# Kernel optimization log

Measured on AMD Instinct MI355X. Metric: run time of the kernel, lower is better.

The kernel has to match this reference:

```python
import jax, jax.numpy as jnp
import numpy as np

B, N, C, H = 4, 1024, 768, 12
D = C // H  # head_dim = 64


def setup_inputs() -> dict:
    key = jax.random.key(0)
    ks = jax.random.split(key, 16)
    def lin(k, fan_in, fan_out):
        # torch Linear init: U(-1/sqrt(fan_in), 1/sqrt(fan_in)); stored as [in, out]
        bound = 1.0 / np.sqrt(fan_in)
        kw, kb = jax.random.split(k)
        W = jax.random.uniform(kw, (fan_in, fan_out), minval=-bound, maxval=bound, dtype=jnp.float32)
        b = jax.random.uniform(kb, (fan_out,), minval=-bound, maxval=bound, dtype=jnp.float32)
        return W, b
    Wq, bq = lin(ks[0], C, C)
    Wk, bk = lin(ks[1], C, C)
    Wv, bv = lin(ks[2], C, C)
    Wo, bo = lin(ks[3], C, C)
    Wd1, bd1 = lin(ks[4], 1, 16)
    Wd2, bd2 = lin(ks[5], 16, H)
    x = jax.random.normal(ks[6], (B, N, C), dtype=jnp.float32)
    coords = jax.random.uniform(ks[7], (B, N, 2), dtype=jnp.float32)
    return {"x": x, "coords": coords,
            "Wq": Wq, "bq": bq, "Wk": Wk, "bk": bk, "Wv": Wv, "bv": bv,
            "Wo": Wo, "bo": bo, "Wd1": Wd1, "bd1": bd1, "Wd2": Wd2, "bd2": bd2}


def reference(x, coords, Wq, bq, Wk, bk, Wv, bv, Wo, bo, Wd1, bd1, Wd2, bd2):
    scale = D ** (-0.5)
    # projections -> [B, H, N, D]
    def heads(t):
        return t.reshape(B, N, H, D).transpose(0, 2, 1, 3)
    q = heads(x @ Wq + bq)
    k = heads(x @ Wk + bk)
    v = heads(x @ Wv + bv)
    # content scores [B, H, N, N]
    content = jnp.einsum('bhid,bhjd->bhij', q, k) * scale
    # pairwise distances [B, N, N, 1]
    diff = coords[:, :, None, :] - coords[:, None, :, :]
    dist = jnp.sqrt(jnp.sum(diff * diff, axis=-1, keepdims=True) + 1e-6)
    # distance MLP: 1 -> 16 -> H, then permute to [B, H, N, N]
    hbias = jax.nn.relu(dist @ Wd1 + bd1)
    spatial = (hbias @ Wd2 + bd2).transpose(0, 3, 1, 2)
    attn = jax.nn.softmax(content + spatial, axis=-1)
    out = jnp.einsum('bhij,bhjd->bhid', attn, v)
    out = out.transpose(0, 2, 1, 3).reshape(B, N, C)
    out = out @ Wo + bo
    return out, attn
```

## Files before the change

### kernel.cpp

```cpp
#include <hip/hip_runtime.h>
#include <cstddef>
#include <cstdint>

#define Bc 4
#define Nc 1024
#define Cc 768
#define Hc 12
#define Dc 64
#define BHc 48
#define QKV_ELEMS ((size_t)Bc * Nc * Cc)

typedef __attribute__((ext_vector_type(4))) unsigned int u32x4;
typedef __attribute__((ext_vector_type(8))) short s16x8;
typedef __attribute__((ext_vector_type(4))) float fx4;
typedef __attribute__((ext_vector_type(2))) float fx2;

union Frag { u32x4 u; s16x8 s; unsigned short h[8]; };

__device__ inline unsigned short f2bf(float x) {
    union { float f; uint32_t u; } c; c.f = x;
    return (unsigned short)((c.u + 0x7FFFu + ((c.u >> 16) & 1u)) >> 16);
}
__device__ inline float bf2f(unsigned short b) {
    union { uint32_t u; float f; } c; c.u = ((uint32_t)b) << 16;
    return c.f;
}
__device__ inline void split8(const float* v, u32x4& hi, u32x4& lo) {
    Frag fh, fl;
    #pragma unroll
    for (int e = 0; e < 8; ++e) {
        const unsigned short hb = f2bf(v[e]);
        fh.h[e] = hb;
        fl.h[e] = f2bf(v[e] - bf2f(hb));
    }
    hi = fh.u; lo = fl.u;
}

__global__ __launch_bounds__(256) void prep_w_kernel(
    const float* __restrict__ Wq, const float* __restrict__ Wk,
    const float* __restrict__ Wv, const float* __restrict__ Wo,
    unsigned short* __restrict__ Thi, unsigned short* __restrict__ Tlo)
{
    __shared__ float scr[64 * 65];
    const int mat = blockIdx.z;
    const float* W = (mat == 0) ? Wq : (mat == 1) ? Wk : (mat == 2) ? Wv : Wo;
    const int k0 = blockIdx.y * 64, n0 = blockIdx.x * 64;
    const int tid = threadIdx.x;

    #pragma unroll
    for (int it = 0; it < 4; ++it) {
        const int lin = tid + it * 256;
        const int r = lin >> 4, c4 = (lin & 15) << 2;
        const fx4 v = *(const fx4*)&W[(size_t)(k0 + r) * 768 + n0 + c4];
        scr[r * 65 + c4 + 0] = v[0]; scr[r * 65 + c4 + 1] = v[1];
        scr[r * 65 + c4 + 2] = v[2]; scr[r * 65 + c4 + 3] = v[3];
    }
    __syncthreads();
    unsigned short* th = Thi + (size_t)mat * 768 * 768;
    unsigned short* tl = Tlo + (size_t)mat * 768 * 768;
    #pragma unroll
    for (int it = 0; it < 16; ++it) {
        const int lin = tid + it * 256;
        const int n = lin >> 6, kq = lin & 63;
        const float val = scr[kq * 65 + n];
        const size_t o = (size_t)(n0 + n) * 768 + k0 + kq;
        const unsigned short hb = f2bf(val);
        th[o] = hb;
        tl[o] = f2bf(val - bf2f(hb));
    }
}

__global__ __launch_bounds__(256) void prep_tables_kernel(
    const float* __restrict__ Wd1, const float* __restrict__ bd1,
    const float* __restrict__ Wd2, const float* __restrict__ bd2,
    float* __restrict__ abPack, float* __restrict__ kact, int* __restrict__ meta)
{
    __shared__ float w1s[16], b1s[16], kn[16];
    __shared__ int rank[16];
    const int tid = threadIdx.x;
    if (tid < 16) {
        const float w1 = Wd1[tid], b1 = bd1[tid];
        w1s[tid] = w1; b1s[tid] = b1;
        kn[tid] = (w1 != 0.0f) ? (-b1 / w1) : INFINITY;
    }
    __syncthreads();
    if (tid < 16) {
        int rk = 0;
        for (int u = 0; u < 16; ++u) {
            const float ku = kn[u], km = kn[tid];
            if (ku < km || (ku == km && u < tid)) ++rk;
        }
        rank[tid] = rk;
    }
    if (tid == 0) {
        int nn = 0, na = 0;
        for (int t = 0; t < 16; ++t) {
            const float kt = kn[t];
            if (kt < 0.00099f) ++nn;
            else if (kt < 1.41422f) kact[na++] = kt;
        }
        meta[0] = nn; meta[1] = na;
    }
    __syncthreads();
    if (tid < 17 * 12) {
        const int s = tid / 12, h = tid % 12;
        float a = 0.0f, be = bd2[h];
        for (int u = 0; u < 16; ++u) {
            const float w1 = w1s[u], b1 = b1s[u];
            bool act;
            if (w1 > 0.0f)      act = (rank[u] < s);
            else if (w1 < 0.0f) act = (rank[u] >= s);
            else                act = (b1 > 0.0f);
            if (act) {
                const float w2 = Wd2[u * 12 + h];
                a  += w2 * w1;
                be += w2 * b1;
            }
        }
        abPack[tid * 2 + 0] = a;
        abPack[tid * 2 + 1] = be;
    }
}

__global__ __launch_bounds__(256) void split_x_kernel(
    const float* __restrict__ x, unsigned short* __restrict__ xhi,
    unsigned short* __restrict__ xlo)
{
    const size_t t = (size_t)blockIdx.x * 256 + threadIdx.x;
    float vv[8];
    const fx4 a = *(const fx4*)&x[t * 8];
    const fx4 b = *(const fx4*)&x[t * 8 + 4];
    vv[0]=a[0]; vv[1]=a[1]; vv[2]=a[2]; vv[3]=a[3];
    vv[4]=b[0]; vv[5]=b[1]; vv[6]=b[2]; vv[7]=b[3];
    u32x4 hi, lo; split8(vv, hi, lo);
    *(u32x4*)&xhi[t * 8] = hi;
    *(u32x4*)&xlo[t * 8] = lo;
}

struct SmemG { u32x4 ah[512]; u32x4 al[512]; u32x4 bh[512]; u32x4 bl[512]; };
struct SmemT { float scr[64 * 68]; };
union SmemU { SmemG g; SmemT t; };

template<int AMODE, int OMODE>
__global__ __launch_bounds__(256) void gemm_mfma_kernel(
    const unsigned short* __restrict__ Ahi, const unsigned short* __restrict__ Alo,
    const float* __restrict__ P0, const float* __restrict__ P1,
    const unsigned short* __restrict__ Bhi, const unsigned short* __restrict__ Blo,
    const float* __restrict__ bias,
    float* __restrict__ outF,
    unsigned short* __restrict__ Ohi, unsigned short* __restrict__ Olo)
{
    __shared__ SmemU sm;
    const int tid = threadIdx.x;
    const int w = tid >> 6, L = tid & 63;
    const int Lr = L & 15, Lg = L >> 4;
    const int m0 = blockIdx.y * 64, n0 = blockIdx.x * 64;

    fx4 acc[2][2] = {};

    for (int kk = 0; kk < 768; kk += 64) {
        #pragma unroll
        for (int it = 0; it < 2; ++it) {
            const int slot = tid + it * 256;
            const int s = slot >> 6, l = slot & 63;
            const int row = m0 + ((s >> 1) << 4) + (l & 15);
            const int kb = kk + ((s & 1) << 5) + ((l >> 4) << 3);
            if (AMODE == 1) {
                sm.g.ah[slot] = *(const u32x4*)&Ahi[(size_t)row * 768 + kb];
                sm.g.al[slot] = *(const u32x4*)&Alo[(size_t)row * 768 + kb];
            } else {
                const fx4 a0 = *(const fx4*)&P0[(size_t)row * 768 + kb];
                const fx4 a1 = *(const fx4*)&P0[(size_t)row * 768 + kb + 4];
                const fx4 c0 = *(const fx4*)&P1[(size_t)row * 768 + kb];
                const fx4 c1 = *(const fx4*)&P1[(size_t)row * 768 + kb + 4];
                float vv[8];
                vv[0]=a0[0]+c0[0]; vv[1]=a0[1]+c0[1]; vv[2]=a0[2]+c0[2]; vv[3]=a0[3]+c0[3];
                vv[4]=a1[0]+c1[0]; vv[5]=a1[1]+c1[1]; vv[6]=a1[2]+c1[2]; vv[7]=a1[3]+c1[3];
                u32x4 hi, lo; split8(vv, hi, lo);
                sm.g.ah[slot] = hi;
                sm.g.al[slot] = lo;
            }
            const int col = n0 + ((s >> 1) << 4) + (l & 63 & 15);
            sm.g.bh[slot] = *(const u32x4*)&Bhi[(size_t)col * 768 + kb];
            sm.g.bl[slot] = *(const u32x4*)&Blo[(size_t)col * 768 + kb];
        }
        __syncthreads();
        #pragma unroll
        for (int kc = 0; kc < 2; ++kc) {
            Frag ah[2], al[2], bh[2], bl[2];
            #pragma unroll
            for (int mm = 0; mm < 2; ++mm) {
                const int rg = (w >> 1) * 2 + mm;
                ah[mm].u = sm.g.ah[(rg * 2 + kc) * 64 + L];
                al[mm].u = sm.g.al[(rg * 2 + kc) * 64 + L];
            }
            #pragma unroll
            for (int nn = 0; nn < 2; ++nn) {
                const int cg = (w & 1) * 2 + nn;
                bh[nn].u = sm.g.bh[(cg * 2 + kc) * 64 + L];
                bl[nn].u = sm.g.bl[(cg * 2 + kc) * 64 + L];
            }
            #pragma unroll
            for (int mm = 0; mm < 2; ++mm)
                #pragma unroll
                for (int nn = 0; nn < 2; ++nn) {
                    acc[mm][nn] = __builtin_amdgcn_mfma_f32_16x16x32_bf16(ah[mm].s, bh[nn].s, acc[mm][nn], 0, 0, 0);
                    acc[mm][nn] = __builtin_amdgcn_mfma_f32_16x16x32_bf16(ah[mm].s, bl[nn].s, acc[mm][nn], 0, 0, 0);
                    acc[mm][nn] = __builtin_amdgcn_mfma_f32_16x16x32_bf16(al[mm].s, bh[nn].s, acc[mm][nn], 0, 0, 0);
                }
        }
        __syncthreads();
    }

    #pragma unroll
    for (int mm = 0; mm < 2; ++mm) {
        const int rl = (w >> 1) * 32 + mm * 16 + Lg * 4;
        #pragma unroll
        for (int nn = 0; nn < 2; ++nn) {
            const int cl = (w & 1) * 32 + nn * 16 + Lr;
            const float bs = bias[n0 + cl];
            #pragma unroll
            for (int r = 0; r < 4; ++r)
                sm.t.scr[(rl + r) * 68 + cl] = acc[mm][nn][r] + bs;
        }
    }
    __syncthreads();

    if (OMODE == 0) {
        const int h = n0 >> 6;
        #pragma unroll
        for (int it = 0; it < 2; ++it) {
            const int t = tid + it * 256;
            const int r = t >> 3, d0 = (t & 7) << 3;
            float vv[8];
            #pragma unroll
            for (int e = 0; e < 8; ++e) vv[e] = sm.t.scr[r * 68 + d0 + e];
            u32x4 hi, lo; split8(vv, hi, lo);
            const int rg = m0 + r, b = rg >> 10, nloc = rg & 1023;
            const size_t o = (((size_t)(b * Hc + h) * Nc + nloc) << 6) + d0;
            *(u32x4*)&Ohi[o] = hi;
            *(u32x4*)&Olo[o] = lo;
        }
    } else if (OMODE == 1) {
        const int b = m0 >> 10, h = n0 >> 6, nbase = m0 & 1023;
        #pragma unroll
        for (int it = 0; it < 2; ++it) {
            const int t = tid + it * 256;
            const int dd = t >> 3, j0 = (t & 7) << 3;
            float vv[8];
            #pragma unroll
            for (int e = 0; e < 8; ++e) vv[e] = sm.t.scr[(j0 + e) * 68 + dd];
            u32x4 hi, lo; split8(vv, hi, lo);
            const size_t o = (size_t)((b * Hc + h) * Dc + dd) * Nc + nbase + j0;
            *(u32x4*)&Ohi[o] = hi;
            *(u32x4*)&Olo[o] = lo;
        }
    } else {
        #pragma unroll
        for (int it = 0; it < 4; ++it) {
            const int lin = tid + it * 256;
            const int r = lin >> 4, c4 = (lin & 15) << 2;
            const fx4 v = *(const fx4*)&sm.t.scr[r * 68 + c4];
            *(fx4*)&outF[(size_t)(m0 + r) * 768 + n0 + c4] = v;
        }
    }
}

__global__ __launch_bounds__(256, 4) void scores_half_kernel(
    const unsigned short* __restrict__ qhi, const unsigned short* __restrict__ qlo,
    const unsigned short* __restrict__ khi, const unsigned short* __restrict__ klo,
    const float* __restrict__ coords,
    const float* __restrict__ abPack, const float* __restrict__ kact,
    const int* __restrict__ meta,
    float* __restrict__ attn, float* __restrict__ ml)
{
    __shared__ u32x4 KsH[512], KsL[512];
    __shared__ fx2 cjs[512];
    __shared__ fx2 abt[17];
    __shared__ float kacts[16];
    __shared__ int metas[2];

    const int tid = threadIdx.x;
    const int w = tid >> 6, L = tid & 63;
    const int Lr = L & 15, Lg = L >> 4;
    const int bh = blockIdx.z, b = bh / Hc, h = bh % Hc;
    const int i0 = blockIdx.x * 64, half = blockIdx.y;
    const int i = i0 + w * 16 + Lr;
    const int Lg4 = Lg * 4;

    if (tid < 17) abt[tid] = *(const fx2*)&abPack[(tid * Hc + h) * 2];
    else if (tid >= 32 && tid < 48) kacts[tid - 32] = kact[tid - 32];
    else if (tid == 64) { metas[0] = meta[0]; metas[1] = meta[1]; }
    for (int t = tid; t < 512; t += 256)
        cjs[t] = *(const fx2*)&coords[((size_t)b * Nc + half * 512 + t) * 2];

    Frag qh[2], ql[2];
    #pragma unroll
    for (int kc = 0; kc < 2; ++kc) {
        const size_t o = ((size_t)bh * Nc + i) * 64 + kc * 32 + Lg * 8;
        qh[kc].u = *(const u32x4*)&qhi[o];
        ql[kc].u = *(const u32x4*)&qlo[o];
    }
    const fx2 ci = *(const fx2*)&coords[((size_t)b * Nc + i) * 2];
    __syncthreads();
    const int n_neg = metas[0], n_act = metas[1];

    float m_r = -INFINITY, l_r = 0.f;
    const size_t rowbase = ((size_t)bh * Nc + i) * Nc + half * 512;

    for (int jt = 0; jt < 8; ++jt) {
        #pragma unroll
        for (int it = 0; it < 2; ++it) {
            const int slot = tid + it * 256;
            const int s = slot >> 6, l = slot & 63;
            const int jrow = half * 512 + jt * 64 + ((s >> 1) << 4) + (l & 15);
            const int kb = ((s & 1) << 5) + ((l >> 4) << 3);
            const size_t o = ((size_t)bh * Nc + jrow) * 64 + kb;
            KsH[slot] = *(const u32x4*)&khi[o];
            KsL[slot] = *(const u32x4*)&klo[o];
        }
        __syncthreads();

        fx4 acc[4] = {};
        #pragma unroll
        for (int kc = 0; kc < 2; ++kc) {
            #pragma unroll
            for (int cg = 0; cg < 4; ++cg) {
                Frag kh_, kl_;
                kh_.u = KsH[(cg * 2 + kc) * 64 + L];
                kl_.u = KsL[(cg * 2 + kc) * 64 + L];
                acc[cg] = __builtin_amdgcn_mfma_f32_16x16x32_bf16(kh_.s, qh[kc].s, acc[cg], 0, 0, 0);
                acc[cg] = __builtin_amdgcn_mfma_f32_16x16x32_bf16(kl_.s, qh[kc].s, acc[cg], 0, 0, 0);
                acc[cg] = __builtin_amdgcn_mfma_f32_16x16x32_bf16(kh_.s, ql[kc].s, acc[cg], 0, 0, 0);
            }
        }

        float sv[16];
        #pragma unroll
        for (int cg = 0; cg < 4; ++cg) {
            float dist4[4]; int idx4[4];
            #pragma unroll
            for (int r = 0; r < 4; ++r) {
                const fx2 cj = cjs[jt * 64 + cg * 16 + Lg4 + r];
                const float dx = ci[0] - cj[0], dy = ci[1] - cj[1];
                dist4[r] = sqrtf(fmaf(dx, dx, fmaf(dy, dy, 1e-6f)));
                idx4[r] = n_neg;
            }
            for (int t = 0; t < n_act; ++t) {
                const float kt = kacts[t];
                #pragma unroll
                for (int r = 0; r < 4; ++r) idx4[r] += (dist4[r] > kt) ? 1 : 0;
            }
            #pragma unroll
            for (int r = 0; r < 4; ++r) {
                const fx2 ab = abt[idx4[r]];
                sv[cg * 4 + r] = fmaf(acc[cg][r], 0.125f, fmaf(ab[0], dist4[r], ab[1]));
            }
        }

        #pragma unroll
        for (int cg = 0; cg < 4; ++cg) {
            fx4 st;
            st[0] = sv[cg*4+0]; st[1] = sv[cg*4+1]; st[2] = sv[cg*4+2]; st[3] = sv[cg*4+3];
            *(fx4*)&attn[rowbase + jt * 64 + cg * 16 + Lg4] = st;
        }

        float tm = sv[0];
        #pragma unroll
        for (int e = 1; e < 16; ++e) tm = fmaxf(tm, sv[e]);
        tm = fmaxf(tm, __shfl_xor(tm, 16));
        tm = fmaxf(tm, __shfl_xor(tm, 32));
        const float mnew = fmaxf(m_r, tm);
        float ts = 0.f;
        #pragma unroll
        for (int e = 0; e < 16; ++e) ts += __expf(sv[e] - mnew);
        ts += __shfl_xor(ts, 16);
        ts += __shfl_xor(ts, 32);
        l_r = l_r * __expf(m_r - mnew) + ts;
        m_r = mnew;
        __syncthreads();
    }

    if (Lg == 0) {
        const size_t mo = (((size_t)bh * Nc + i) * 2 + half) * 2;
        ml[mo + 0] = m_r;
        ml[mo + 1] = l_r;
    }
}

__global__ __launch_bounds__(256, 4) void pv_half_kernel(
    float* __restrict__ attn,
    const unsigned short* __restrict__ vThi, const unsigned short* __restrict__ vTlo,
    const float* __restrict__ ml,
    float* __restrict__ Hp)
{
    __shared__ u32x4 VsH[512], VsL[512];
    const int tid = threadIdx.x;
    const int w = tid >> 6, L = tid & 63;
    const int Lr = L & 15, Lg = L >> 4;
    const int bh = blockIdx.z, b = bh / Hc, h = bh % Hc;
    const int i0 = blockIdx.x * 64, half = blockIdx.y;
    const int wrow = i0 + w * 16;

    const size_t prow = (size_t)bh * Nc + wrow + Lr;
    const fx4 m4 = *(const fx4*)&ml[prow * 4];
    const float mm = fmaxf(m4[0], m4[2]);
    const float ll = m4[1] * __expf(m4[0] - mm) + m4[3] * __expf(m4[2] - mm);
    const float il = 1.0f / ll;

    fx4 acc[4] = {};

    for (int jt = 0; jt < 8; ++jt) {
        const int jglob = half * 8 + jt;
        #pragma unroll
        for (int it = 0; it < 2; ++it) {
            const int slot = tid + it * 256;
            const int s = slot >> 6, l = slot & 63;
            const int dd = ((s >> 1) << 4) + (l & 15);
            const int j = jglob * 64 + ((s & 1) << 5) + ((l >> 4) << 3);
            const size_t o = ((size_t)bh * Dc + dd) * Nc + j;
            VsH[slot] = *(const u32x4*)&vThi[o];
            VsL[slot] = *(const u32x4*)&vTlo[o];
        }
        __syncthreads();

        #pragma unroll
        for (int kc = 0; kc < 2; ++kc) {
            float* ap = &attn[prow * Nc + jglob * 64 + kc * 32 + Lg * 8];
            const fx4 s0 = *(const fx4*)ap;
            const fx4 s1 = *(const fx4*)(ap + 4);
            float p[8];
            p[0] = __expf(s0[0] - mm) * il; p[1] = __expf(s0[1] - mm) * il;
            p[2] = __expf(s0[2] - mm) * il; p[3] = __expf(s0[3] - mm) * il;
            p[4] = __expf(s1[0] - mm) * il; p[5] = __expf(s1[1] - mm) * il;
            p[6] = __expf(s1[2] - mm) * il; p[7] = __expf(s1[3] - mm) * il;
            fx4 w0, w1;
            w0[0]=p[0]; w0[1]=p[1]; w0[2]=p[2]; w0[3]=p[3];
            w1[0]=p[4]; w1[1]=p[5]; w1[2]=p[6]; w1[3]=p[7];
            *(fx4*)ap = w0;
            *(fx4*)(ap + 4) = w1;
            u32x4 phi, plo; split8(p, phi, plo);
            Frag ph, pl; ph.u = phi; pl.u = plo;
            #pragma unroll
            for (int dg = 0; dg < 4; ++dg) {
                Frag vh, vl;
                vh.u = VsH[(dg * 2 + kc) * 64 + L];
                vl.u = VsL[(dg * 2 + kc) * 64 + L];
                acc[dg] = __builtin_amdgcn_mfma_f32_16x16x32_bf16(ph.s, vh.s, acc[dg], 0, 0, 0);
                acc[dg] = __builtin_amdgcn_mfma_f32_16x16x32_bf16(ph.s, vl.s, acc[dg], 0, 0, 0);
                acc[dg] = __builtin_amdgcn_mfma_f32_16x16x32_bf16(pl.s, vh.s, acc[dg], 0, 0, 0);
            }
        }
        __syncthreads();
    }

    #pragma unroll
    for (int dg = 0; dg < 4; ++dg)
        #pragma unroll
        for (int r = 0; r < 4; ++r) {
            const int irow = wrow + Lg * 4 + r;
            Hp[(size_t)half * QKV_ELEMS + ((size_t)b * Nc + irow) * Cc + h * Dc + dg * 16 + Lr]
                = acc[dg][r];
        }
}

extern "C" void kernel_launch(void* const* d_in, const int* in_sizes, int n_in,
                              void* d_out, int out_size, void* d_ws, size_t ws_size,
                              hipStream_t stream)
{
    (void)in_sizes; (void)n_in; (void)out_size; (void)ws_size;

    const float* x      = (const float*)d_in[0];
    const float* coords = (const float*)d_in[1];
    const float* Wq = (const float*)d_in[2];  const float* bq = (const float*)d_in[3];
    const float* Wk = (const float*)d_in[4];  const float* bk = (const float*)d_in[5];
    const float* Wv = (const float*)d_in[6];  const float* bv = (const float*)d_in[7];
    const float* Wo = (const float*)d_in[8];  const float* bo = (const float*)d_in[9];
    const float* Wd1 = (const float*)d_in[10]; const float* bd1 = (const float*)d_in[11];
    const float* Wd2 = (const float*)d_in[12]; const float* bd2 = (const float*)d_in[13];

    float* out_main = (float*)d_out;
    float* attn     = out_main + QKV_ELEMS;

    uint8_t* wsb = (uint8_t*)d_ws;
    const size_t SZ_BF = (size_t)BHc * Nc * Dc * 2;
    const size_t SZ_W4 = (size_t)4 * 768 * 768 * 2;
    unsigned short* qhi  = (unsigned short*)(wsb + 0 * SZ_BF);
    unsigned short* qlo  = (unsigned short*)(wsb + 1 * SZ_BF);
    unsigned short* khi  = (unsigned short*)(wsb + 2 * SZ_BF);
    unsigned short* klo  = (unsigned short*)(wsb + 3 * SZ_BF);
    unsigned short* vThi = (unsigned short*)(wsb + 4 * SZ_BF);
    unsigned short* vTlo = (unsigned short*)(wsb + 5 * SZ_BF);
    float*          Hp   = (float*)(wsb + 0 * SZ_BF);
    unsigned short* xhi  = (unsigned short*)(wsb + 6 * SZ_BF);
    unsigned short* xlo  = (unsigned short*)(wsb + 7 * SZ_BF);
    unsigned short* Thi  = (unsigned short*)(wsb + 8 * SZ_BF);
    unsigned short* Tlo  = (unsigned short*)(wsb + 8 * SZ_BF + SZ_W4);
    float* mlbuf  = (float*)(wsb + 8 * SZ_BF + 2 * SZ_W4);
    float* abPack = mlbuf + (size_t)BHc * Nc * 4;
    float* kact   = abPack + 17 * 12 * 2;
    int*   meta   = (int*)(kact + 16);

    prep_w_kernel<<<dim3(12, 12, 4), 256, 0, stream>>>(Wq, Wk, Wv, Wo, Thi, Tlo);
    prep_tables_kernel<<<1, 256, 0, stream>>>(Wd1, bd1, Wd2, bd2, abPack, kact, meta);
    split_x_kernel<<<dim3(1536), 256, 0, stream>>>(x, xhi, xlo);

    dim3 gGemm(12, 64);
    gemm_mfma_kernel<1, 0><<<gGemm, 256, 0, stream>>>(
        xhi, xlo, nullptr, nullptr, Thi + (size_t)0 * 768 * 768, Tlo + (size_t)0 * 768 * 768,
        bq, nullptr, qhi, qlo);
    gemm_mfma_kernel<1, 0><<<gGemm, 256, 0, stream>>>(
        xhi, xlo, nullptr, nullptr, Thi + (size_t)1 * 768 * 768, Tlo + (size_t)1 * 768 * 768,
        bk, nullptr, khi, klo);
    gemm_mfma_kernel<1, 1><<<gGemm, 256, 0, stream>>>(
        xhi, xlo, nullptr, nullptr, Thi + (size_t)2 * 768 * 768, Tlo + (size_t)2 * 768 * 768,
        bv, nullptr, vThi, vTlo);

    scores_half_kernel<<<dim3(16, 2, 48), 256, 0, stream>>>(
        qhi, qlo, khi, klo, coords, abPack, kact, meta, attn, mlbuf);

    pv_half_kernel<<<dim3(16, 2, 48), 256, 0, stream>>>(
        attn, vThi, vTlo, mlbuf, Hp);

    gemm_mfma_kernel<2, 2><<<gGemm, 256, 0, stream>>>(
        nullptr, nullptr, Hp, Hp + QKV_ELEMS, Thi + (size_t)3 * 768 * 768,
        Tlo + (size_t)3 * 768 * 768, bo, out_main, nullptr, nullptr);
}
```

Measured before the change: 404.6 us.

## Store per-tile exponentials, LUT spline bins, and reduce PV halves in-block

The scores kernel now writes exp(s - tile_max) with per-64-column tile max and sum stats instead of raw scores. The pv kernel then only rescales by a per-tile factor, which removes its exp work. Spline segment lookup is replaced by a 2048-entry byte LUT built in the prep kernel, and K/V tiles are loaded directly into registers instead of staged through LDS. The PV kernel combines its two column halves in shared memory and writes a bf16 hi/lo split of the head output, so the output GEMM loads split operands directly. Risks are LUT binning errors near knot boundaries and less memory reuse without LDS staging.

```diff
diff --git a/kernel.cpp b/kernel.cpp
--- a/kernel.cpp
+++ b/kernel.cpp
@@ -73,7 +73,7 @@
 __global__ __launch_bounds__(256) void prep_tables_kernel(
     const float* __restrict__ Wd1, const float* __restrict__ bd1,
     const float* __restrict__ Wd2, const float* __restrict__ bd2,
-    float* __restrict__ abPack, float* __restrict__ kact, int* __restrict__ meta)
+    float* __restrict__ abPack, unsigned char* __restrict__ lut)
 {
     __shared__ float w1s[16], b1s[16], kn[16];
     __shared__ int rank[16];
@@ -91,15 +91,6 @@
             if (ku < km || (ku == km && u < tid)) ++rk;
         }
         rank[tid] = rk;
-    }
-    if (tid == 0) {
-        int nn = 0, na = 0;
-        for (int t = 0; t < 16; ++t) {
-            const float kt = kn[t];
-            if (kt < 0.00099f) ++nn;
-            else if (kt < 1.41422f) kact[na++] = kt;
-        }
-        meta[0] = nn; meta[1] = na;
     }
     __syncthreads();
     if (tid < 17 * 12) {
@@ -120,6 +111,12 @@
         abPack[tid * 2 + 0] = a;
         abPack[tid * 2 + 1] = be;
     }
+    for (int b = tid; b < 2048; b += 256) {
+        const float rep = (b + 0.5f) * (1.41422f / 2048.0f);
+        int cnt = 0;
+        for (int t = 0; t < 16; ++t) cnt += (rep > kn[t]) ? 1 : 0;
+        lut[b] = (unsigned char)cnt;
+    }
 }
 
 __global__ __launch_bounds__(256) void split_x_kernel(
@@ -141,10 +138,9 @@
 struct SmemT { float scr[64 * 68]; };
 union SmemU { SmemG g; SmemT t; };
 
-template<int AMODE, int OMODE>
+template<int OMODE>
 __global__ __launch_bounds__(256) void gemm_mfma_kernel(
     const unsigned short* __restrict__ Ahi, const unsigned short* __restrict__ Alo,
-    const float* __restrict__ P0, const float* __restrict__ P1,
     const unsigned short* __restrict__ Bhi, const unsigned short* __restrict__ Blo,
     const float* __restrict__ bias,
     float* __restrict__ outF,
@@ -165,22 +161,9 @@
             const int s = slot >> 6, l = slot & 63;
             const int row = m0 + ((s >> 1) << 4) + (l & 15);
             const int kb = kk + ((s & 1) << 5) + ((l >> 4) << 3);
-            if (AMODE == 1) {
-                sm.g.ah[slot] = *(const u32x4*)&Ahi[(size_t)row * 768 + kb];
-                sm.g.al[slot] = *(const u32x4*)&Alo[(size_t)row * 768 + kb];
-            } else {
-                const fx4 a0 = *(const fx4*)&P0[(size_t)row * 768 + kb];
-                const fx4 a1 = *(const fx4*)&P0[(size_t)row * 768 + kb + 4];
-                const fx4 c0 = *(const fx4*)&P1[(size_t)row * 768 + kb];
-                const fx4 c1 = *(const fx4*)&P1[(size_t)row * 768 + kb + 4];
-                float vv[8];
-                vv[0]=a0[0]+c0[0]; vv[1]=a0[1]+c0[1]; vv[2]=a0[2]+c0[2]; vv[3]=a0[3]+c0[3];
-                vv[4]=a1[0]+c1[0]; vv[5]=a1[1]+c1[1]; vv[6]=a1[2]+c1[2]; vv[7]=a1[3]+c1[3];
-                u32x4 hi, lo; split8(vv, hi, lo);
-                sm.g.ah[slot] = hi;
-                sm.g.al[slot] = lo;
-            }
-            const int col = n0 + ((s >> 1) << 4) + (l & 63 & 15);
+            sm.g.ah[slot] = *(const u32x4*)&Ahi[(size_t)row * 768 + kb];
+            sm.g.al[slot] = *(const u32x4*)&Alo[(size_t)row * 768 + kb];
+            const int col = n0 + ((s >> 1) << 4) + (l & 15);
             sm.g.bh[slot] = *(const u32x4*)&Bhi[(size_t)col * 768 + kb];
             sm.g.bl[slot] = *(const u32x4*)&Blo[(size_t)col * 768 + kb];
         }
@@ -266,19 +249,16 @@
     }
 }
 
-__global__ __launch_bounds__(256, 4) void scores_half_kernel(
+__global__ __launch_bounds__(256) void scores_kernel(
     const unsigned short* __restrict__ qhi, const unsigned short* __restrict__ qlo,
     const unsigned short* __restrict__ khi, const unsigned short* __restrict__ klo,
     const float* __restrict__ coords,
-    const float* __restrict__ abPack, const float* __restrict__ kact,
-    const int* __restrict__ meta,
-    float* __restrict__ attn, float* __restrict__ ml)
-{
-    __shared__ u32x4 KsH[512], KsL[512];
+    const float* __restrict__ abPack, const unsigned char* __restrict__ lutg,
+    float* __restrict__ attn, float* __restrict__ mlf)
+{
+    __shared__ fx2 abt[17];
+    __shared__ unsigned char luts[2048];
     __shared__ fx2 cjs[512];
-    __shared__ fx2 abt[17];
-    __shared__ float kacts[16];
-    __shared__ int metas[2];
 
     const int tid = threadIdx.x;
     const int w = tid >> 6, L = tid & 63;
@@ -288,11 +268,12 @@
     const int i = i0 + w * 16 + Lr;
     const int Lg4 = Lg * 4;
 
-    if (tid < 17) abt[tid] = *(const fx2*)&abPack[(tid * Hc + h) * 2];
-    else if (tid >= 32 && tid < 48) kacts[tid - 32] = kact[tid - 32];
-    else if (tid == 64) { metas[0] = meta[0]; metas[1] = meta[1]; }
-    for (int t = tid; t < 512; t += 256)
+    if (tid < 17) abt[tid] = ((const fx2*)abPack)[tid * Hc + h];
+    #pragma unroll
+    for (int t = tid; t < 512; t += 256) {
+        ((uint32_t*)luts)[t] = ((const uint32_t*)lutg)[t];
         cjs[t] = *(const fx2*)&coords[((size_t)b * Nc + half * 512 + t) * 2];
+    }
 
     Frag qh[2], ql[2];
     #pragma unroll
@@ -303,165 +284,163 @@
     }
     const fx2 ci = *(const fx2*)&coords[((size_t)b * Nc + i) * 2];
     __syncthreads();
-    const int n_neg = metas[0], n_act = metas[1];
-
-    float m_r = -INFINITY, l_r = 0.f;
+
     const size_t rowbase = ((size_t)bh * Nc + i) * Nc + half * 512;
+    const size_t mlbase = ((size_t)bh * Nc + i) * 16 + half * 8;
 
     for (int jt = 0; jt < 8; ++jt) {
-        #pragma unroll
-        for (int it = 0; it < 2; ++it) {
-            const int slot = tid + it * 256;
-            const int s = slot >> 6, l = slot & 63;
-            const int jrow = half * 512 + jt * 64 + ((s >> 1) << 4) + (l & 15);
-            const int kb = ((s & 1) << 5) + ((l >> 4) << 3);
-            const size_t o = ((size_t)bh * Nc + jrow) * 64 + kb;
-            KsH[slot] = *(const u32x4*)&khi[o];
-            KsL[slot] = *(const u32x4*)&klo[o];
-        }
-        __syncthreads();
+        const int jbase = half * 512 + jt * 64;
 
         fx4 acc[4] = {};
         #pragma unroll
         for (int kc = 0; kc < 2; ++kc) {
+            Frag kh[4], kl[4];
             #pragma unroll
             for (int cg = 0; cg < 4; ++cg) {
-                Frag kh_, kl_;
-                kh_.u = KsH[(cg * 2 + kc) * 64 + L];
-                kl_.u = KsL[(cg * 2 + kc) * 64 + L];
-                acc[cg] = __builtin_amdgcn_mfma_f32_16x16x32_bf16(kh_.s, qh[kc].s, acc[cg], 0, 0, 0);
-                acc[cg] = __builtin_amdgcn_mfma_f32_16x16x32_bf16(kl_.s, qh[kc].s, acc[cg], 0, 0, 0);
-                acc[cg] = __builtin_amdgcn_mfma_f32_16x16x32_bf16(kh_.s, ql[kc].s, acc[cg], 0, 0, 0);
+                const size_t o = ((size_t)bh * Nc + jbase + cg * 16 + Lr) * 64 + kc * 32 + Lg * 8;
+                kh[cg].u = *(const u32x4*)&khi[o];
+                kl[cg].u = *(const u32x4*)&klo[o];
+            }
+            #pragma unroll
+            for (int cg = 0; cg < 4; ++cg) {
+                acc[cg] = __builtin_amdgcn_mfma_f32_16x16x32_bf16(kh[cg].s, qh[kc].s, acc[cg], 0, 0, 0);
+                acc[cg] = __builtin_amdgcn_mfma_f32_16x16x32_bf16(kl[cg].s, qh[kc].s, acc[cg], 0, 0, 0);
+                acc[cg] = __builtin_amdgcn_mfma_f32_16x16x32_bf16(kh[cg].s, ql[kc].s, acc[cg], 0, 0, 0);
             }
         }
 
         float sv[16];
         #pragma unroll
         for (int cg = 0; cg < 4; ++cg) {
-            float dist4[4]; int idx4[4];
             #pragma unroll
             for (int r = 0; r < 4; ++r) {
                 const fx2 cj = cjs[jt * 64 + cg * 16 + Lg4 + r];
                 const float dx = ci[0] - cj[0], dy = ci[1] - cj[1];
-                dist4[r] = sqrtf(fmaf(dx, dx, fmaf(dy, dy, 1e-6f)));
-                idx4[r] = n_neg;
-            }
-            for (int t = 0; t < n_act; ++t) {
-                const float kt = kacts[t];
-                #pragma unroll
-                for (int r = 0; r < 4; ++r) idx4[r] += (dist4[r] > kt) ? 1 : 0;
-            }
-            #pragma unroll
-            for (int r = 0; r < 4; ++r) {
-                const fx2 ab = abt[idx4[r]];
-                sv[cg * 4 + r] = fmaf(acc[cg][r], 0.125f, fmaf(ab[0], dist4[r], ab[1]));
-            }
-        }
-
+                const float dist = sqrtf(fmaf(dx, dx, fmaf(dy, dy, 1e-6f)));
+                int bin = (int)(dist * (2048.0f / 1.41422f));
+                bin = (bin > 2047) ? 2047 : bin;
+                const fx2 ab = abt[luts[bin]];
+                sv[cg * 4 + r] = fmaf(acc[cg][r], 0.125f, fmaf(ab[0], dist, ab[1]));
+            }
+        }
+
+        float tm = sv[0];
+        #pragma unroll
+        for (int e = 1; e < 16; ++e) tm = fmaxf(tm, sv[e]);
+        tm = fmaxf(tm, __shfl_xor(tm, 16));
+        tm = fmaxf(tm, __shfl_xor(tm, 32));
+
+        float ts = 0.f;
+        #pragma unroll
+        for (int e = 0; e < 16; ++e) { sv[e] = __expf(sv[e] - tm); ts += sv[e]; }
         #pragma unroll
         for (int cg = 0; cg < 4; ++cg) {
             fx4 st;
             st[0] = sv[cg*4+0]; st[1] = sv[cg*4+1]; st[2] = sv[cg*4+2]; st[3] = sv[cg*4+3];
             *(fx4*)&attn[rowbase + jt * 64 + cg * 16 + Lg4] = st;
         }
-
-        float tm = sv[0];
-        #pragma unroll
-        for (int e = 1; e < 16; ++e) tm = fmaxf(tm, sv[e]);
-        tm = fmaxf(tm, __shfl_xor(tm, 16));
-        tm = fmaxf(tm, __shfl_xor(tm, 32));
-        const float mnew = fmaxf(m_r, tm);
-        float ts = 0.f;
-        #pragma unroll
-        for (int e = 0; e < 16; ++e) ts += __expf(sv[e] - mnew);
         ts += __shfl_xor(ts, 16);
         ts += __shfl_xor(ts, 32);
-        l_r = l_r * __expf(m_r - mnew) + ts;
-        m_r = mnew;
-        __syncthreads();
-    }
-
-    if (Lg == 0) {
-        const size_t mo = (((size_t)bh * Nc + i) * 2 + half) * 2;
-        ml[mo + 0] = m_r;
-        ml[mo + 1] = l_r;
-    }
-}
-
-__global__ __launch_bounds__(256, 4) void pv_half_kernel(
+        if (Lg == 0) {
+            *(fx2*)&mlf[(mlbase + jt) * 2] = fx2{tm, ts};
+        }
+    }
+}
+
+__global__ __launch_bounds__(256) void pv_kernel(
     float* __restrict__ attn,
     const unsigned short* __restrict__ vThi, const unsigned short* __restrict__ vTlo,
-    const float* __restrict__ ml,
-    float* __restrict__ Hp)
-{
-    __shared__ u32x4 VsH[512], VsL[512];
+    const float* __restrict__ mlf,
+    unsigned short* __restrict__ Hphi, unsigned short* __restrict__ Hplo)
+{
+    __shared__ float accs[32 * 64];
     const int tid = threadIdx.x;
     const int w = tid >> 6, L = tid & 63;
     const int Lr = L & 15, Lg = L >> 4;
-    const int bh = blockIdx.z, b = bh / Hc, h = bh % Hc;
-    const int i0 = blockIdx.x * 64, half = blockIdx.y;
-    const int wrow = i0 + w * 16;
-
-    const size_t prow = (size_t)bh * Nc + wrow + Lr;
-    const fx4 m4 = *(const fx4*)&ml[prow * 4];
-    const float mm = fmaxf(m4[0], m4[2]);
-    const float ll = m4[1] * __expf(m4[0] - mm) + m4[3] * __expf(m4[2] - mm);
-    const float il = 1.0f / ll;
+    const int wr = w >> 1, wc = w & 1;
+    const int bh = blockIdx.y, b = bh / Hc, h = bh % Hc;
+    const int i0 = blockIdx.x * 32;
+    const int row = i0 + wr * 16 + Lr;
+
+    const float* mlr = &mlf[((size_t)bh * Nc + row) * 32];
+    float mt[16], lt[16];
+    #pragma unroll
+    for (int t = 0; t < 8; ++t) {
+        const fx4 v = *(const fx4*)&mlr[t * 4];
+        mt[t*2+0] = v[0]; lt[t*2+0] = v[1];
+        mt[t*2+1] = v[2]; lt[t*2+1] = v[3];
+    }
+    float m_row = mt[0];
+    #pragma unroll
+    for (int t = 1; t < 16; ++t) m_row = fmaxf(m_row, mt[t]);
+    float l_row = 0.f;
+    #pragma unroll
+    for (int t = 0; t < 16; ++t) l_row = fmaf(lt[t], __expf(mt[t] - m_row), l_row);
+    const float il = 1.0f / l_row;
 
     fx4 acc[4] = {};
+    const size_t arow = ((size_t)bh * Nc + row) * Nc;
 
     for (int jt = 0; jt < 8; ++jt) {
-        const int jglob = half * 8 + jt;
-        #pragma unroll
-        for (int it = 0; it < 2; ++it) {
-            const int slot = tid + it * 256;
-            const int s = slot >> 6, l = slot & 63;
-            const int dd = ((s >> 1) << 4) + (l & 15);
-            const int j = jglob * 64 + ((s & 1) << 5) + ((l >> 4) << 3);
-            const size_t o = ((size_t)bh * Dc + dd) * Nc + j;
-            VsH[slot] = *(const u32x4*)&vThi[o];
-            VsL[slot] = *(const u32x4*)&vTlo[o];
-        }
-        __syncthreads();
-
+        const int jbase = wc * 512 + jt * 64;
+        const float f = __expf(mlr[(wc * 8 + jt) * 2] - m_row) * il;
         #pragma unroll
         for (int kc = 0; kc < 2; ++kc) {
-            float* ap = &attn[prow * Nc + jglob * 64 + kc * 32 + Lg * 8];
+            float* ap = &attn[arow + jbase + kc * 32 + Lg * 8];
             const fx4 s0 = *(const fx4*)ap;
             const fx4 s1 = *(const fx4*)(ap + 4);
             float p[8];
-            p[0] = __expf(s0[0] - mm) * il; p[1] = __expf(s0[1] - mm) * il;
-            p[2] = __expf(s0[2] - mm) * il; p[3] = __expf(s0[3] - mm) * il;
-            p[4] = __expf(s1[0] - mm) * il; p[5] = __expf(s1[1] - mm) * il;
-            p[6] = __expf(s1[2] - mm) * il; p[7] = __expf(s1[3] - mm) * il;
+            p[0]=s0[0]*f; p[1]=s0[1]*f; p[2]=s0[2]*f; p[3]=s0[3]*f;
+            p[4]=s1[0]*f; p[5]=s1[1]*f; p[6]=s1[2]*f; p[7]=s1[3]*f;
             fx4 w0, w1;
             w0[0]=p[0]; w0[1]=p[1]; w0[2]=p[2]; w0[3]=p[3];
             w1[0]=p[4]; w1[1]=p[5]; w1[2]=p[6]; w1[3]=p[7];
             *(fx4*)ap = w0;
             *(fx4*)(ap + 4) = w1;
-            u32x4 phi, plo; split8(p, phi, plo);
-            Frag ph, pl; ph.u = phi; pl.u = plo;
+            u32x4 phiu, plou; split8(p, phiu, plou);
+            Frag ph, pl; ph.u = phiu; pl.u = plou;
+
+            Frag vh[4], vl[4];
             #pragma unroll
             for (int dg = 0; dg < 4; ++dg) {
-                Frag vh, vl;
-                vh.u = VsH[(dg * 2 + kc) * 64 + L];
-                vl.u = VsL[(dg * 2 + kc) * 64 + L];
-                acc[dg] = __builtin_amdgcn_mfma_f32_16x16x32_bf16(ph.s, vh.s, acc[dg], 0, 0, 0);
-                acc[dg] = __builtin_amdgcn_mfma_f32_16x16x32_bf16(ph.s, vl.s, acc[dg], 0, 0, 0);
-                acc[dg] = __builtin_amdgcn_mfma_f32_16x16x32_bf16(pl.s, vh.s, acc[dg], 0, 0, 0);
-            }
-        }
-        __syncthreads();
-    }
-
-    #pragma unroll
-    for (int dg = 0; dg < 4; ++dg)
-        #pragma unroll
-        for (int r = 0; r < 4; ++r) {
-            const int irow = wrow + Lg * 4 + r;
-            Hp[(size_t)half * QKV_ELEMS + ((size_t)b * Nc + irow) * Cc + h * Dc + dg * 16 + Lr]
-                = acc[dg][r];
-        }
+                const size_t o = ((size_t)bh * Dc + dg * 16 + Lr) * Nc + jbase + kc * 32 + Lg * 8;
+                vh[dg].u = *(const u32x4*)&vThi[o];
+                vl[dg].u = *(const u32x4*)&vTlo[o];
+            }
+            #pragma unroll
+            for (int dg = 0; dg < 4; ++dg) {
+                acc[dg] = __builtin_amdgcn_mfma_f32_16x16x32_bf16(ph.s, vh[dg].s, acc[dg], 0, 0, 0);
+                acc[dg] = __builtin_amdgcn_mfma_f32_16x16x32_bf16(ph.s, vl[dg].s, acc[dg], 0, 0, 0);
+                acc[dg] = __builtin_amdgcn_mfma_f32_16x16x32_bf16(pl.s, vh[dg].s, acc[dg], 0, 0, 0);
+            }
+        }
+    }
+
+    if (wc == 0) {
+        #pragma unroll
+        for (int dg = 0; dg < 4; ++dg)
+            #pragma unroll
+            for (int r = 0; r < 4; ++r)
+                accs[(wr * 16 + Lg * 4 + r) * 64 + dg * 16 + Lr] = acc[dg][r];
+    }
+    __syncthreads();
+    if (wc == 1) {
+        #pragma unroll
+        for (int dg = 0; dg < 4; ++dg)
+            #pragma unroll
+            for (int r = 0; r < 4; ++r)
+                accs[(wr * 16 + Lg * 4 + r) * 64 + dg * 16 + Lr] += acc[dg][r];
+    }
+    __syncthreads();
+
+    const int r2 = tid >> 3, d0 = (tid & 7) << 3;
+    float vv[8];
+    #pragma unroll
+    for (int e = 0; e < 8; ++e) vv[e] = accs[r2 * 64 + d0 + e];
+    u32x4 hi, lo; split8(vv, hi, lo);
+    const size_t o = ((size_t)b * Nc + i0 + r2) * Cc + h * Dc + d0;
+    *(u32x4*)&Hphi[o] = hi;
+    *(u32x4*)&Hplo[o] = lo;
 }
 
 extern "C" void kernel_launch(void* const* d_in, const int* in_sizes, int n_in,
@@ -491,38 +470,36 @@
     unsigned short* klo  = (unsigned short*)(wsb + 3 * SZ_BF);
     unsigned short* vThi = (unsigned short*)(wsb + 4 * SZ_BF);
     unsigned short* vTlo = (unsigned short*)(wsb + 5 * SZ_BF);
-    float*          Hp   = (float*)(wsb + 0 * SZ_BF);
     unsigned short* xhi  = (unsigned short*)(wsb + 6 * SZ_BF);
     unsigned short* xlo  = (unsigned short*)(wsb + 7 * SZ_BF);
     unsigned short* Thi  = (unsigned short*)(wsb + 8 * SZ_BF);
     unsigned short* Tlo  = (unsigned short*)(wsb + 8 * SZ_BF + SZ_W4);
     float* mlbuf  = (float*)(wsb + 8 * SZ_BF + 2 * SZ_W4);
-    float* abPack = mlbuf + (size_t)BHc * Nc * 4;
-    float* kact   = abPack + 17 * 12 * 2;
-    int*   meta   = (int*)(kact + 16);
+    float* abPack = mlbuf + (size_t)BHc * Nc * 32;
+    unsigned char* lut = (unsigned char*)(abPack + 17 * 12 * 2);
 
     prep_w_kernel<<<dim3(12, 12, 4), 256, 0, stream>>>(Wq, Wk, Wv, Wo, Thi, Tlo);
-    prep_tables_kernel<<<1, 256, 0, stream>>>(Wd1, bd1, Wd2, bd2, abPack, kact, meta);
+    prep_tables_kernel<<<1, 256, 0, stream>>>(Wd1, bd1, Wd2, bd2, abPack, lut);
     split_x_kernel<<<dim3(1536), 256, 0, stream>>>(x, xhi, xlo);
 
     dim3 gGemm(12, 64);
-    gemm_mfma_kernel<1, 0><<<gGemm, 256, 0, stream>>>(
-        xhi, xlo, nullptr, nullptr, Thi + (size_t)0 * 768 * 768, Tlo + (size_t)0 * 768 * 768,
+    gemm_mfma_kernel<0><<<gGemm, 256, 0, stream>>>(
+        xhi, xlo, Thi + (size_t)0 * 768 * 768, Tlo + (size_t)0 * 768 * 768,
         bq, nullptr, qhi, qlo);
-    gemm_mfma_kernel<1, 0><<<gGemm, 256, 0, stream>>>(
-        xhi, xlo, nullptr, nullptr, Thi + (size_t)1 * 768 * 768, Tlo + (size_t)1 * 768 * 768,
+    gemm_mfma_kernel<0><<<gGemm, 256, 0, stream>>>(
+        xhi, xlo, Thi + (size_t)1 * 768 * 768, Tlo + (size_t)1 * 768 * 768,
         bk, nullptr, khi, klo);
-    gemm_mfma_kernel<1, 1><<<gGemm, 256, 0, stream>>>(
-        xhi, xlo, nullptr, nullptr, Thi + (size_t)2 * 768 * 768, Tlo + (size_t)2 * 768 * 768,
+    gemm_mfma_kernel<1><<<gGemm, 256, 0, stream>>>(
+        xhi, xlo, Thi + (size_t)2 * 768 * 768, Tlo + (size_t)2 * 768 * 768,
         bv, nullptr, vThi, vTlo);
 
-    scores_half_kernel<<<dim3(16, 2, 48), 256, 0, stream>>>(
-        qhi, qlo, khi, klo, coords, abPack, kact, meta, attn, mlbuf);
-
-    pv_half_kernel<<<dim3(16, 2, 48), 256, 0, stream>>>(
-        attn, vThi, vTlo, mlbuf, Hp);
-
-    gemm_mfma_kernel<2, 2><<<gGemm, 256, 0, stream>>>(
-        nullptr, nullptr, Hp, Hp + QKV_ELEMS, Thi + (size_t)3 * 768 * 768,
-        Tlo + (size_t)3 * 768 * 768, bo, out_main, nullptr, nullptr);
-}
+    scores_kernel<<<dim3(16, 2, 48), 256, 0, stream>>>(
+        qhi, qlo, khi, klo, coords, abPack, lut, attn, mlbuf);
+
+    pv_kernel<<<dim3(32, 48), 256, 0, stream>>>(
+        attn, vThi, vTlo, mlbuf, xhi, xlo);
+
+    gemm_mfma_kernel<2><<<gGemm, 256, 0, stream>>>(
+        xhi, xlo, Thi + (size_t)3 * 768 * 768, Tlo + (size_t)3 * 768 * 768,
+        bo, out_main, nullptr, nullptr);
+}
```

Measured after the change: 453.4 us. 12.1% more time.
